# Optimization experiments

Hardware: AMD Instinct MI355X
Metric: run time of the kernel (lower is better)

The kernel has to match this reference:

```python
import jax, jax.numpy as jnp
import numpy as np

L = 2048           # lattice side
R = 2.777          # public-goods multiplier r
GAMMA = 0.8
ETA = 0.8
K_FERMI = 0.5      # fermi temperature used in fermiUpdate


def _plus_sum(x):
    """3x3 plus-kernel conv with circular (wrap) padding == self + 4 rolled neighbors."""
    return (x
            + jnp.roll(x, 1, 0) + jnp.roll(x, -1, 0)
            + jnp.roll(x, 1, 1) + jnp.roll(x, -1, 1))


def setup_inputs() -> dict:
    key = jax.random.key(0)
    k1, k2, k3, k4, k5 = jax.random.split(key, 5)
    return {
        "type_t_minus": jax.random.randint(k1, (L, L), 0, 2, dtype=jnp.int32),
        "type_t": jax.random.randint(k2, (L, L), 0, 2, dtype=jnp.int32),
        "Q_tensor": jax.random.normal(k3, (L * L, 2, 2), dtype=jnp.float32),
        "learning_direction": jax.random.randint(k4, (L, L), 0, 4, dtype=jnp.int32),
        "learning_probabilities": jax.random.uniform(k5, (L, L), dtype=jnp.float32),
    }


def reference(type_t_minus, type_t, Q_tensor, learning_direction, learning_probabilities):
    N = L * L
    # ---- calculation_value: per-cell payoff from the 5 overlapping PGG games ----
    c = (type_t == 1).astype(jnp.float32)   # cooperator mask
    d = (type_t == 0).astype(jnp.float32)   # defector mask
    coop_num = _plus_sum(c)                  # cooperators in own 5-cell group
    base = coop_num * (R / 5.0)
    profit = _plus_sum(base - 1.0) * c + _plus_sum(base) * d   # [L, L]

    # ---- updateQMatrix: Q[C, A, B] <- (1-eta)*Q[C,A,B] + eta*(profit + gamma*max_b Q[C,B,b]) ----
    A = type_t_minus.reshape(-1)             # previous action, [N]
    B = type_t.reshape(-1)                   # current action,  [N]
    Qb = jnp.take_along_axis(Q_tensor, B[:, None, None], axis=1)[:, 0, :]  # Q[C, B, :] -> [N, 2]
    max_values = Qb.max(axis=1)              # [N]
    flatQ = Q_tensor.reshape(N, 4)
    idx = A * 2 + B                          # flattened (A, B) index
    old = jnp.take_along_axis(flatQ, idx[:, None], axis=1)[:, 0]
    upd = (1.0 - ETA) * old + ETA * (profit.reshape(-1) + GAMMA * max_values)
    Q_new = flatQ.at[jnp.arange(N), idx].set(upd).reshape(N, 2, 2)

    # ---- fermiUpdate: gather just-updated Q[C,A,B] (== upd), compare with 4 neighbors ----
    pm = upd.reshape(L, L)                   # fermi profit matrix

    def W(shift, axis):
        return 1.0 / (1.0 + jnp.exp((pm - jnp.roll(pm, shift, axis)) / K_FERMI))

    Ws = jnp.stack([W(1, 1), W(-1, 1), W(1, 0), W(-1, 0)])        # left,right,up,down [4,L,L]
    nb = jnp.stack([jnp.roll(type_t, 1, 1), jnp.roll(type_t, -1, 1),
                    jnp.roll(type_t, 1, 0), jnp.roll(type_t, -1, 0)])
    W_sel = jnp.take_along_axis(Ws, learning_direction[None], axis=0)[0]
    nb_sel = jnp.take_along_axis(nb, learning_direction[None], axis=0)[0]
    type_t1 = jnp.where(learning_probabilities <= W_sel, nb_sel, type_t)  # [L, L] int32

    return (Q_new, type_t1, profit)
```

## Files before the change

### kernel.cpp

```cpp
#include <hip/hip_runtime.h>


#define LSIDE 2048
#define LMASK 2047
#define LSHIFT 11
#define NCELL (LSIDE * LSIDE)

__global__ __launch_bounds__(256) void spgg_fused(
    const int* __restrict__ tmin,
    const int* __restrict__ tt,
    const float* __restrict__ Q,
    const int* __restrict__ ldir,
    const float* __restrict__ lp,
    float* __restrict__ Qn,
    float* __restrict__ prof,
    float* __restrict__ t1out)
{
    __shared__ int tile[4][7][72];

    const int tid = threadIdx.x;
    const int w   = tid >> 6;
    const int l   = tid & 63;
    const int idx = blockIdx.x * 256 + tid;
    const int i   = idx >> LSHIFT;
    const int j   = idx & LMASK;
    const int j0w = j & ~63;

    {
        const int base_row = i - 3;
        const int base_col = j0w - 4;
#pragma unroll
        for (int p = 0; p < 2; ++p) {
            int k = l + (p << 6);
            if (k < 126) {
                int r = (k * 57) >> 10;
                int m = k - r * 18;
                int rg = (base_row + r) & LMASK;
                int cg = (base_col + (m << 2)) & LMASK;
                int4 v = *(const int4*)&tt[(rg << LSHIFT) + cg];
                *(int4*)&tile[w][r][m << 2] = v;
            }
        }
    }

    float4 qr = ((const float4*)Q)[idx];
    int    A  = tmin[idx];
    int    dir = ldir[idx];
    float  pv  = lp[idx];

    int di = (dir == 3) - (dir == 2);
    int dj = (dir == 1) - (dir == 0);
    int ni = (i + di) & LMASK;
    int nj = (j + dj) & LMASK;
    int nidx = (ni << LSHIFT) + nj;

    float4 qn4 = ((const float4*)Q)[nidx];
    int    An  = tmin[nidx];

    const float KB        = 0.5554f;
    const float ETA       = 0.8f;
    const float ONE_M_ETA = 0.2f;
    const float GAMMA     = 0.8f;

#define M(r, c) (tile[w][r][c] == 1)

    auto profit_at = [&](int r, int c) -> float {
        int m_cc = M(r, c);
        int cn_c = m_cc + M(r-1, c) + M(r+1, c) + M(r, c-1) + M(r, c+1);
        int cn_u = M(r-1, c) + M(r-2, c) + m_cc + M(r-1, c-1) + M(r-1, c+1);
        int cn_d = M(r+1, c) + m_cc + M(r+2, c) + M(r+1, c-1) + M(r+1, c+1);
        int cn_l = M(r, c-1) + M(r-1, c-1) + M(r+1, c-1) + M(r, c-2) + m_cc;
        int cn_r = M(r, c+1) + M(r-1, c+1) + M(r+1, c+1) + m_cc + M(r, c+2);
        float b_c = __fmul_rn((float)cn_c, KB);
        float b_u = __fmul_rn((float)cn_u, KB);
        float b_d = __fmul_rn((float)cn_d, KB);
        float b_l = __fmul_rn((float)cn_l, KB);
        float b_r = __fmul_rn((float)cn_r, KB);
        float s0 = __fadd_rn(__fadd_rn(__fadd_rn(__fadd_rn(b_c, b_u), b_d), b_l), b_r);
        float s1 = __fadd_rn(__fadd_rn(__fadd_rn(__fadd_rn(
                       __fsub_rn(b_c, 1.0f), __fsub_rn(b_u, 1.0f)),
                       __fsub_rn(b_d, 1.0f)), __fsub_rn(b_l, 1.0f)),
                       __fsub_rn(b_r, 1.0f));
        return m_cc ? s1 : s0;
    };

    auto upd_of = [&](float profit, float4 q4, int Ax, int Bx) -> float {
        float q0 = (Bx == 0) ? q4.x : q4.z;
        float q1 = (Bx == 0) ? q4.y : q4.w;
        float mx = fmaxf(q0, q1);
        int k = Ax * 2 + Bx;
        float old = (k == 0) ? q4.x : ((k == 1) ? q4.y : ((k == 2) ? q4.z : q4.w));
        float t0 = __fmul_rn(GAMMA, mx);
        float t1 = __fadd_rn(profit, t0);
        float t2 = __fmul_rn(ETA, t1);
        float t3 = __fmul_rn(ONE_M_ETA, old);
        return __fadd_rn(t3, t2);
    };

    const int lr = 3, lc = l + 4;

    float p_own = profit_at(lr, lc);
    int B = tile[w][lr][lc];
    float upd = upd_of(p_own, qr, A, B);

    int k = A * 2 + B;
    float4 qo;
    qo.x = (k == 0) ? upd : qr.x;
    qo.y = (k == 1) ? upd : qr.y;
    qo.z = (k == 2) ? upd : qr.z;
    qo.w = (k == 3) ? upd : qr.w;
    ((float4*)Qn)[idx] = qo;
    prof[idx] = p_own;

    float p_nb = profit_at(lr + di, lc + dj);
    int Bn = tile[w][lr + di][lc + dj];
    float upd_nb = upd_of(p_nb, qn4, An, Bn);

    float e1 = __fsub_rn(upd, upd_nb);
    float e2 = __fmul_rn(e1, 2.0f);
    float ex = (float)exp((double)e2);
    float W  = __fdiv_rn(1.0f, __fadd_rn(1.0f, ex));
    int sel = (pv <= W) ? Bn : B;
    t1out[idx] = (float)sel;
#undef M
}

extern "C" void kernel_launch(void* const* d_in, const int* in_sizes, int n_in,
                              void* d_out, int out_size, void* d_ws, size_t ws_size,
                              hipStream_t stream) {
    const int*   type_t_minus = (const int*)d_in[0];
    const int*   type_t       = (const int*)d_in[1];
    const float* Q_tensor     = (const float*)d_in[2];
    const int*   ldir         = (const int*)d_in[3];
    const float* lprob        = (const float*)d_in[4];

    float* out   = (float*)d_out;
    float* Qn    = out;
    float* t1out = out + (size_t)4 * NCELL;
    float* prof  = out + (size_t)5 * NCELL;

    const int threads = 256;
    const int blocks  = NCELL / threads;
    spgg_fused<<<blocks, threads, 0, stream>>>(type_t_minus, type_t, Q_tensor,
                                               ldir, lprob, Qn, prof, t1out);
}
```

Baseline: 218.3 us.

## Replace LDS tile with wavefront ballot bitmasks and profit lookup table

Removes the shared-memory tile of the cooperator field. Each wavefront now reads 7 rows directly and packs cooperator masks with __ballot, then spreads each 7-bit window into nibbles so that group counts become packed integer adds. Profit becomes a lookup into a 64K-entry float table that a small extra kernel precomputes every call. This avoids LDS traffic and the per-cell floating-point sums, at the cost of an extra launch, a workspace table, and scattered gather loads from it.

```diff
diff --git a/kernel.cpp b/kernel.cpp
--- a/kernel.cpp
+++ b/kernel.cpp
@@ -6,104 +6,141 @@
 #define LSHIFT 11
 #define NCELL (LSIDE * LSIDE)
 
+__global__ __launch_bounds__(256) void spgg_lut_init(float* __restrict__ lut) {
+    int idx = blockIdx.x * 256 + threadIdx.x;
+    int cn_c = idx & 7;
+    int cn_u = (idx >> 3) & 7;
+    int cn_d = (idx >> 6) & 7;
+    int cn_l = (idx >> 9) & 7;
+    int cn_r = (idx >> 12) & 7;
+    int ccc  = (idx >> 15) & 1;
+    const float KB = 0.5554f;
+    float b_c = __fmul_rn((float)cn_c, KB);
+    float b_u = __fmul_rn((float)cn_u, KB);
+    float b_d = __fmul_rn((float)cn_d, KB);
+    float b_l = __fmul_rn((float)cn_l, KB);
+    float b_r = __fmul_rn((float)cn_r, KB);
+    float s0 = __fadd_rn(__fadd_rn(__fadd_rn(__fadd_rn(b_c, b_u), b_d), b_l), b_r);
+    float s1 = __fadd_rn(__fadd_rn(__fadd_rn(__fadd_rn(
+                   __fsub_rn(b_c, 1.0f), __fsub_rn(b_u, 1.0f)),
+                   __fsub_rn(b_d, 1.0f)), __fsub_rn(b_l, 1.0f)),
+                   __fsub_rn(b_r, 1.0f));
+    lut[idx] = ccc ? s1 : s0;
+}
+
 __global__ __launch_bounds__(256) void spgg_fused(
     const int* __restrict__ tmin,
     const int* __restrict__ tt,
     const float* __restrict__ Q,
     const int* __restrict__ ldir,
     const float* __restrict__ lp,
+    const float* __restrict__ lut,
     float* __restrict__ Qn,
     float* __restrict__ prof,
     float* __restrict__ t1out)
 {
-    __shared__ int tile[4][7][72];
-
     const int tid = threadIdx.x;
-    const int w   = tid >> 6;
     const int l   = tid & 63;
     const int idx = blockIdx.x * 256 + tid;
     const int i   = idx >> LSHIFT;
     const int j   = idx & LMASK;
     const int j0w = j & ~63;
 
-    {
-        const int base_row = i - 3;
-        const int base_col = j0w - 4;
-#pragma unroll
-        for (int p = 0; p < 2; ++p) {
-            int k = l + (p << 6);
-            if (k < 126) {
-                int r = (k * 57) >> 10;
-                int m = k - r * 18;
-                int rg = (base_row + r) & LMASK;
-                int cg = (base_col + (m << 2)) & LMASK;
-                int4 v = *(const int4*)&tt[(rg << LSHIFT) + cg];
-                *(int4*)&tile[w][r][m << 2] = v;
-            }
-        }
-    }
-
-    float4 qr = ((const float4*)Q)[idx];
-    int    A  = tmin[idx];
+    float4 qr  = ((const float4*)Q)[idx];
+    int    A   = tmin[idx];
     int    dir = ldir[idx];
     float  pv  = lp[idx];
 
+    unsigned long long hm;
+    {
+        int hv = 0;
+        int o  = l % 6;
+        int hr = l / 6;
+        if (l < 42) {
+            int col = (j0w + ((o < 3) ? (o - 3) : (o + 61))) & LMASK;
+            int row = (i + hr - 3) & LMASK;
+            hv = tt[(row << LSHIFT) + col];
+        }
+        hm = __ballot(l < 42 && hv == 1);
+    }
+
+    unsigned int E[7];
+#pragma unroll
+    for (int r = 0; r < 7; ++r) {
+        int row = (i + r - 3) & LMASK;
+        int v = tt[(row << LSHIFT) + j0w + l];
+        unsigned long long mm = __ballot(v == 1);
+        unsigned int h6 = (unsigned int)((hm >> (6 * r)) & 63ull);
+        unsigned long long lo = (mm << 3) | (unsigned long long)(h6 & 7u);
+        unsigned long long hi = (mm >> 29) | ((unsigned long long)(h6 >> 3) << 35);
+        unsigned int win = (unsigned int)(((l < 58) ? (lo >> l) : (hi >> (l - 32))) & 0x7Full);
+        unsigned int x = win;
+        x = (x | (x << 12)) & 0x0007000Fu;
+        x = (x | (x << 6))  & 0x03030303u;
+        x = (x | (x << 3))  & 0x11111111u;
+        E[r] = x;
+    }
+
+    unsigned int C[5];
+#pragma unroll
+    for (int r = 0; r < 5; ++r) {
+        unsigned int e = E[r + 1];
+        C[r] = E[r] + e + E[r + 2] + (e << 4) + (e >> 4);
+    }
+
+    unsigned int cn_c = (C[2] >> 12) & 7u;
+    unsigned int cn_u = (C[1] >> 12) & 7u;
+    unsigned int cn_d = (C[3] >> 12) & 7u;
+    unsigned int cn_l = (C[2] >> 8)  & 7u;
+    unsigned int cn_r = (C[2] >> 16) & 7u;
+    unsigned int mcc  = (E[3] >> 12) & 1u;
+    unsigned int io   = cn_c | (cn_u << 3) | (cn_d << 6) | (cn_l << 9)
+                      | (cn_r << 12) | (mcc << 15);
+    float p_own = lut[io];
+
     int di = (dir == 3) - (dir == 2);
     int dj = (dir == 1) - (dir == 0);
-    int ni = (i + di) & LMASK;
-    int nj = (j + dj) & LMASK;
-    int nidx = (ni << LSHIFT) + nj;
-
+    int nidx = (((i + di) & LMASK) << LSHIFT) + ((j + dj) & LMASK);
     float4 qn4 = ((const float4*)Q)[nidx];
     int    An  = tmin[nidx];
 
-    const float KB        = 0.5554f;
+    unsigned int Ca = (di < 0) ? C[0] : ((di > 0) ? C[2] : C[1]);
+    unsigned int Cb = (di < 0) ? C[1] : ((di > 0) ? C[3] : C[2]);
+    unsigned int Cc = (di < 0) ? C[2] : ((di > 0) ? C[4] : C[3]);
+    unsigned int Eb = (di < 0) ? E[2] : ((di > 0) ? E[4] : E[3]);
+    int sh = 4 * dj + 12;
+    unsigned int cnc_n = (Cb >> sh) & 7u;
+    unsigned int cnu_n = (Ca >> sh) & 7u;
+    unsigned int cnd_n = (Cc >> sh) & 7u;
+    unsigned int cnl_n = (Cb >> (sh - 4)) & 7u;
+    unsigned int cnr_n = (Cb >> (sh + 4)) & 7u;
+    unsigned int mnb   = (Eb >> sh) & 1u;
+    unsigned int in_   = cnc_n | (cnu_n << 3) | (cnd_n << 6) | (cnl_n << 9)
+                       | (cnr_n << 12) | (mnb << 15);
+    float p_nb = lut[in_];
+
     const float ETA       = 0.8f;
     const float ONE_M_ETA = 0.2f;
     const float GAMMA     = 0.8f;
+    int B  = (int)mcc;
+    int Bn = (int)mnb;
 
-#define M(r, c) (tile[w][r][c] == 1)
+    float q0 = (B == 0) ? qr.x : qr.z;
+    float q1 = (B == 0) ? qr.y : qr.w;
+    float mx = fmaxf(q0, q1);
+    int k = A * 2 + B;
+    float old = (k == 0) ? qr.x : ((k == 1) ? qr.y : ((k == 2) ? qr.z : qr.w));
+    float upd = __fadd_rn(__fmul_rn(ONE_M_ETA, old),
+                          __fmul_rn(ETA, __fadd_rn(p_own, __fmul_rn(GAMMA, mx))));
 
-    auto profit_at = [&](int r, int c) -> float {
-        int m_cc = M(r, c);
-        int cn_c = m_cc + M(r-1, c) + M(r+1, c) + M(r, c-1) + M(r, c+1);
-        int cn_u = M(r-1, c) + M(r-2, c) + m_cc + M(r-1, c-1) + M(r-1, c+1);
-        int cn_d = M(r+1, c) + m_cc + M(r+2, c) + M(r+1, c-1) + M(r+1, c+1);
-        int cn_l = M(r, c-1) + M(r-1, c-1) + M(r+1, c-1) + M(r, c-2) + m_cc;
-        int cn_r = M(r, c+1) + M(r-1, c+1) + M(r+1, c+1) + m_cc + M(r, c+2);
-        float b_c = __fmul_rn((float)cn_c, KB);
-        float b_u = __fmul_rn((float)cn_u, KB);
-        float b_d = __fmul_rn((float)cn_d, KB);
-        float b_l = __fmul_rn((float)cn_l, KB);
-        float b_r = __fmul_rn((float)cn_r, KB);
-        float s0 = __fadd_rn(__fadd_rn(__fadd_rn(__fadd_rn(b_c, b_u), b_d), b_l), b_r);
-        float s1 = __fadd_rn(__fadd_rn(__fadd_rn(__fadd_rn(
-                       __fsub_rn(b_c, 1.0f), __fsub_rn(b_u, 1.0f)),
-                       __fsub_rn(b_d, 1.0f)), __fsub_rn(b_l, 1.0f)),
-                       __fsub_rn(b_r, 1.0f));
-        return m_cc ? s1 : s0;
-    };
+    float nq0 = (Bn == 0) ? qn4.x : qn4.z;
+    float nq1 = (Bn == 0) ? qn4.y : qn4.w;
+    float nmx = fmaxf(nq0, nq1);
+    int kn = An * 2 + Bn;
+    float nold = (kn == 0) ? qn4.x : ((kn == 1) ? qn4.y : ((kn == 2) ? qn4.z : qn4.w));
+    float upd_nb = __fadd_rn(__fmul_rn(ONE_M_ETA, nold),
+                             __fmul_rn(ETA, __fadd_rn(p_nb, __fmul_rn(GAMMA, nmx))));
 
-    auto upd_of = [&](float profit, float4 q4, int Ax, int Bx) -> float {
-        float q0 = (Bx == 0) ? q4.x : q4.z;
-        float q1 = (Bx == 0) ? q4.y : q4.w;
-        float mx = fmaxf(q0, q1);
-        int k = Ax * 2 + Bx;
-        float old = (k == 0) ? q4.x : ((k == 1) ? q4.y : ((k == 2) ? q4.z : q4.w));
-        float t0 = __fmul_rn(GAMMA, mx);
-        float t1 = __fadd_rn(profit, t0);
-        float t2 = __fmul_rn(ETA, t1);
-        float t3 = __fmul_rn(ONE_M_ETA, old);
-        return __fadd_rn(t3, t2);
-    };
-
-    const int lr = 3, lc = l + 4;
-
-    float p_own = profit_at(lr, lc);
-    int B = tile[w][lr][lc];
-    float upd = upd_of(p_own, qr, A, B);
-
-    int k = A * 2 + B;
     float4 qo;
     qo.x = (k == 0) ? upd : qr.x;
     qo.y = (k == 1) ? upd : qr.y;
@@ -112,17 +149,12 @@
     ((float4*)Qn)[idx] = qo;
     prof[idx] = p_own;
 
-    float p_nb = profit_at(lr + di, lc + dj);
-    int Bn = tile[w][lr + di][lc + dj];
-    float upd_nb = upd_of(p_nb, qn4, An, Bn);
-
     float e1 = __fsub_rn(upd, upd_nb);
     float e2 = __fmul_rn(e1, 2.0f);
     float ex = (float)exp((double)e2);
     float W  = __fdiv_rn(1.0f, __fadd_rn(1.0f, ex));
     int sel = (pv <= W) ? Bn : B;
     t1out[idx] = (float)sel;
-#undef M
 }
 
 extern "C" void kernel_launch(void* const* d_in, const int* in_sizes, int n_in,
@@ -138,9 +170,10 @@
     float* Qn    = out;
     float* t1out = out + (size_t)4 * NCELL;
     float* prof  = out + (size_t)5 * NCELL;
+    float* lut   = (float*)d_ws;
 
-    const int threads = 256;
-    const int blocks  = NCELL / threads;
-    spgg_fused<<<blocks, threads, 0, stream>>>(type_t_minus, type_t, Q_tensor,
-                                               ldir, lprob, Qn, prof, t1out);
+    spgg_lut_init<<<256, 256, 0, stream>>>(lut);
+    spgg_fused<<<NCELL / 256, 256, 0, stream>>>(type_t_minus, type_t, Q_tensor,
+                                                ldir, lprob, lut,
+                                                Qn, prof, t1out);
 }
```

New measurement: 246.4 us. 12.9% more time.
